# Kernel tuning notes

Hardware: AMD Instinct MI355X
Metric: run time of the kernel (lower is better)

The kernel has to match this reference:

```python
import jax, jax.numpy as jnp
import numpy as np
from jax import lax
import math

B, CH, BINS, CROP = 8, 2, 1024, 1024
NUM_BANDS = 4
FF = 2048
EPS = 1e-5
SCALE = 0.02  # weight init scale for numeric stability


def _inorm(x, g, b):
    # InstanceNorm2d: x [B, C, H, W], normalize over (H, W) per (B, C); biased var
    m = x.mean(axis=(2, 3), keepdims=True)
    v = x.var(axis=(2, 3), keepdims=True)
    return (x - m) / jnp.sqrt(v + EPS) * g[None, :, None, None] + b[None, :, None, None]


def _dwconv(x, k):
    # depthwise conv1d: x [B, bins, W], k [bins, 1, 3], padding=1, groups=bins
    return lax.conv_general_dilated(x, k, (1,), [(1, 1)],
                                    dimension_numbers=('NCH', 'OIH', 'NCH'),
                                    feature_group_count=x.shape[1])


def setup_inputs() -> dict:
    key = jax.random.key(0)
    ks = jax.random.split(key, 12)
    inp = {
        'x': jax.random.normal(ks[0], (B, CH, BINS, CROP), jnp.float32),
        'prev_qk': jax.random.normal(ks[1], (B, NUM_BANDS, CROP, CROP), jnp.float32),
        'g_in': jnp.ones((CROP,), jnp.float32),
        'b_in': jnp.zeros((CROP,), jnp.float32),
        'W_in': jax.random.normal(ks[2], (1, CH), jnp.float32) * SCALE,
        'bias_in': jnp.zeros((1,), jnp.float32),
        'g1': jnp.ones((CROP,), jnp.float32),
        'b1': jnp.zeros((CROP,), jnp.float32),
        'Wq': jax.random.normal(ks[3], (BINS, BINS), jnp.float32) * SCALE,
        'Wk': jax.random.normal(ks[4], (BINS, BINS), jnp.float32) * SCALE,
        'Wv': jax.random.normal(ks[5], (BINS, BINS), jnp.float32) * SCALE,
        'Wo': jax.random.normal(ks[6], (BINS, BINS), jnp.float32) * SCALE,
        'kq': jax.random.normal(ks[7], (BINS, 1, 3), jnp.float32) * SCALE,
        'kk': jax.random.normal(ks[8], (BINS, 1, 3), jnp.float32) * SCALE,
        'kv': jax.random.normal(ks[9], (BINS, 1, 3), jnp.float32) * SCALE,
        'pos_w': jax.random.normal(ks[10], (BINS // NUM_BANDS, CROP), jnp.float32) * SCALE,
        'g2': jnp.ones((CROP,), jnp.float32),
        'b2': jnp.zeros((CROP,), jnp.float32),
        'W_ff': jax.random.normal(ks[11], (1, 2), jnp.float32) * SCALE,
        'bias_ff': jnp.zeros((1,), jnp.float32),
        'W1': jax.random.normal(jax.random.fold_in(key, 100), (FF, BINS), jnp.float32) * SCALE,
        'W2': jax.random.normal(jax.random.fold_in(key, 101), (BINS, FF), jnp.float32) * SCALE,
    }
    return inp


def reference(x, prev_qk, g_in, b_in, W_in, bias_in, g1, b1, Wq, Wk, Wv, Wo,
              kq, kk, kv, pos_w, g2, b2, W_ff, bias_ff, W1, W2):
    b = x.shape[0]
    nb = NUM_BANDS
    hd = BINS // nb
    # in_norm + in_project: transposed layout [B, CROP, BINS, CH]
    xt = jnp.transpose(x, (0, 3, 2, 1))
    xt = _inorm(xt, g_in, b_in)
    xt = jnp.einsum('bwhc,oc->bwho', xt, W_in) + bias_in  # [B,CROP,BINS,1]
    x0 = jnp.transpose(xt, (0, 3, 2, 1))                  # [B,1,BINS,CROP]
    # norm1 + attention over frames (w == CROP, c == BINS)
    h = jnp.transpose(_inorm(jnp.transpose(x0, (0, 3, 2, 1)), g1, b1), (0, 3, 2, 1))
    a_in = jnp.transpose(h, (0, 3, 2, 1))[..., 0]         # [B, W, BINS]
    q = jnp.einsum('bwc,oc->bwo', a_in, Wq)
    q = jnp.transpose(_dwconv(jnp.transpose(q, (0, 2, 1)), kq), (0, 2, 1))
    k = jnp.einsum('bwc,oc->bwo', a_in, Wk)
    k = jnp.transpose(_dwconv(jnp.transpose(k, (0, 2, 1)), kk), (0, 2, 1))
    v = jnp.einsum('bwc,oc->bwo', a_in, Wv)
    v = jnp.transpose(_dwconv(jnp.transpose(v, (0, 2, 1)), kv), (0, 2, 1))
    q4 = jnp.transpose(q.reshape(b, CROP, nb, hd), (0, 2, 1, 3))   # [B,nb,W,hd]
    k4 = jnp.transpose(k.reshape(b, CROP, nb, hd), (0, 2, 3, 1))   # [B,nb,hd,W]
    v4 = jnp.transpose(v.reshape(b, CROP, nb, hd), (0, 2, 1, 3))   # [B,nb,W,hd]
    # relative-position bias via pad-and-shift
    p = jnp.matmul(q4, pos_w)                                      # [B,nb,W,CROP]
    p = jnp.pad(p, ((0, 0), (0, 0), (0, 0), (1, 0)))
    p = jnp.swapaxes(p, 2, 3)[:, :, 1:, :]                         # [B,nb,CROP,W]
    qk = (jnp.matmul(q4, k4) + p) / math.sqrt(BINS)
    qk = qk + prev_qk
    a = jax.nn.softmax(qk, axis=-1)
    o = jnp.transpose(jnp.matmul(a, v4), (0, 2, 1, 3)).reshape(b, CROP, BINS)
    o = jnp.einsum('bwc,oc->bwo', o, Wo)                           # [B,W,BINS]
    h4 = jnp.transpose(o[..., None], (0, 3, 2, 1))                 # [B,1,BINS,CROP]
    x1 = jnp.concatenate([x0, h4], axis=1)                         # [B,2,BINS,CROP]
    # norm2 + ff_project + squared-ReLU FFN
    hn = _inorm(jnp.transpose(x1, (0, 3, 2, 1)), g2, b2)           # [B,CROP,BINS,2]
    hn = jnp.einsum('bwhc,oc->bwho', hn, W_ff) + bias_ff           # [B,CROP,BINS,1]
    hn = jnp.transpose(hn, (0, 3, 2, 1))                           # [B,1,BINS,CROP]
    ht = jnp.swapaxes(hn, 2, 3)                                    # [B,1,CROP,BINS]
    ht = jnp.square(jax.nn.relu(jnp.einsum('bowc,fc->bowf', ht, W1)))
    ht = jnp.einsum('bowf,cf->bowc', ht, W2)
    hf = jnp.swapaxes(ht, 2, 3)                                    # [B,1,BINS,CROP]
    out = jnp.concatenate([x1, hf], axis=1)                        # [B,3,BINS,CROP]
    return out, qk
```

## Files before the change

### kernel.cpp

```cpp
#include <hip/hip_runtime.h>
#include <stdint.h>

#define DEVI __device__ __forceinline__

typedef __attribute__((ext_vector_type(8))) short bf16x8;
typedef __attribute__((ext_vector_type(4))) float f32x4;

#define B_    8
#define CROP_ 1024
#define BINS_ 1024
#define NB_   4
#define HD_   256
#define FF_   2048
#define EPSF  1e-5f
#define OUT0_ELEMS (8ull*3ull*1024ull*1024ull)
#define MBYTE (1024ull*1024ull)
#define M1ELEM (1024ll*1024ll)
#define SMCAP 8.0f

DEVI unsigned short f2bf(float f) {
  unsigned u = __builtin_bit_cast(unsigned, f);
  u += 0x7fffu + ((u >> 16) & 1u);
  return (unsigned short)(u >> 16);
}
DEVI float bf2f(unsigned short h) {
  unsigned u = ((unsigned)h) << 16;
  return __builtin_bit_cast(float, u);
}

DEVI void gload16(const unsigned short* g, unsigned short* l) {
  __builtin_amdgcn_global_load_lds(
      (const __attribute__((address_space(1))) unsigned int*)g,
      (__attribute__((address_space(3))) unsigned int*)l, 16, 0, 0);
}

__global__ __launch_bounds__(256) void k_conv_all(
    const float* __restrict__ Wq, const float* __restrict__ Wk,
    const float* __restrict__ Wv, const float* __restrict__ Wo,
    const float* __restrict__ W1, const float* __restrict__ W2,
    const float* __restrict__ pw,
    unsigned short* __restrict__ WQKVB, unsigned short* __restrict__ WOB,
    unsigned short* __restrict__ W1B, unsigned short* __restrict__ W2B,
    unsigned short* __restrict__ PWT) {
  long long i = (long long)blockIdx.x*256 + threadIdx.x;
  long long stride = (long long)gridDim.x*256;
  const long long total = 8*M1ELEM + (1 << 18);
  for (; i < total; i += stride) {
    if (i < 3*M1ELEM) {
      const float* s = i < M1ELEM ? Wq : (i < 2*M1ELEM ? Wk : Wv);
      WQKVB[i] = f2bf(s[i & (M1ELEM-1)]);
    } else if (i < 4*M1ELEM) { WOB[i-3*M1ELEM] = f2bf(Wo[i-3*M1ELEM]); }
    else if (i < 6*M1ELEM)   { W1B[i-4*M1ELEM] = f2bf(W1[i-4*M1ELEM]); }
    else if (i < 8*M1ELEM)   { W2B[i-6*M1ELEM] = f2bf(W2[i-6*M1ELEM]); }
    else {
      long long j = i - 8*M1ELEM;
      int w = (int)(j >> 8), d = (int)(j & 255);
      PWT[j] = f2bf(pw[d*1024 + w]);
    }
  }
}

__global__ __launch_bounds__(256) void k_instx0(const float* __restrict__ x,
    const float* __restrict__ g_in, const float* __restrict__ b_in,
    const float* __restrict__ W_in, const float* __restrict__ bias_in,
    const float* __restrict__ g1, const float* __restrict__ b1,
    float* __restrict__ outp, float* __restrict__ x0t,
    unsigned short* __restrict__ ain) {
  int b = blockIdx.y, w0 = blockIdx.x*32;
  int t = threadIdx.x, wl = t & 31, p = t >> 5;
  const float* xb = x + (size_t)b*2*M1ELEM + w0 + wl;
  float s = 0.f, ss = 0.f;
  for (int i = p*256; i < p*256 + 256; ++i) {
    float v = xb[(size_t)i*CROP_];
    s += v; ss += v*v;
  }
  __shared__ float ls[8][32], lss[8][32];
  __shared__ float s_coef[32], s_add[32];
  __shared__ float s_cm[32], s_ca[32];
  ls[p][wl] = s; lss[p][wl] = ss;
  __syncthreads();
  float W0 = W_in[0], W1 = W_in[1], bi = bias_in[0];
  float sW = W0 + W1;
  if (t < 32) {
    float S = 0.f, SS = 0.f;
    for (int q = 0; q < 8; ++q) { S += ls[q][t]; SS += lss[q][t]; }
    float m = S*(1.f/2048.f);
    float var = SS*(1.f/2048.f) - m*m;
    float r = rsqrtf(var + EPSF);
    int w = w0 + t;
    float coef = r*g_in[w];
    s_coef[t] = coef;
    s_add[t] = b_in[w]*sW + bi - coef*m*sW;
  }
  __syncthreads();
  __shared__ float tile[32][33];
  int tx = wl, ty = p;
  float coef = s_coef[tx], add = s_add[tx];
  int w = w0 + tx;
  float s1 = 0.f, ss1 = 0.f;
  for (int h0 = 0; h0 < BINS_; h0 += 32) {
#pragma unroll
    for (int q = 0; q < 4; ++q) {
      int h = h0 + ty + q*8;
      size_t i0 = ((size_t)b*2*BINS_ + h)*CROP_ + w;
      float val = coef*(W0*x[i0] + W1*x[i0 + (size_t)M1ELEM]) + add;
      outp[(((size_t)b*3)*BINS_ + h)*CROP_ + w] = val;
      tile[ty + q*8][tx] = val;
      s1 += val; ss1 += val*val;
    }
    __syncthreads();
#pragma unroll
    for (int q = 0; q < 4; ++q)
      x0t[((size_t)b*CROP_ + w0 + ty + q*8)*BINS_ + h0 + tx] = tile[tx][ty + q*8];
    __syncthreads();
  }
  ls[p][wl] = s1; lss[p][wl] = ss1;
  __syncthreads();
  if (t < 32) {
    float S = 0.f, SS = 0.f;
    for (int q = 0; q < 8; ++q) { S += ls[q][t]; SS += lss[q][t]; }
    float m = S*(1.f/1024.f);
    float var = SS*(1.f/1024.f) - m*m;
    float rs = rsqrtf(var + EPSF);
    int ww = w0 + t;
    float cm = rs*g1[ww];
    s_cm[t] = cm;
    s_ca[t] = b1[ww] - m*cm;
  }
  __syncthreads();
  for (int wloc = 0; wloc < 32; ++wloc) {
    float cm = s_cm[wloc], ca = s_ca[wloc];
    const float* row = x0t + ((size_t)b*CROP_ + w0 + wloc)*BINS_;
    float4 v = *(const float4*)&row[t*4];
    ushort4 o;
    o.x = f2bf(v.x*cm + ca);
    o.y = f2bf(v.y*cm + ca);
    o.z = f2bf(v.z*cm + ca);
    o.w = f2bf(v.w*cm + ca);
    *(ushort4*)&ain[((size_t)b*CROP_ + w0 + wloc)*BINS_ + t*4] = o;
  }
}

__global__ __launch_bounds__(256) void k_norm2(const float* __restrict__ x0t,
    const float* __restrict__ o2,
    const float* __restrict__ g2, const float* __restrict__ b2,
    const float* __restrict__ W_ff, const float* __restrict__ bias_ff,
    unsigned short* __restrict__ hn) {
  int r = blockIdx.x;
  int w = r & (CROP_ - 1);
  int t = threadIdx.x;
  const float* ra = x0t + (size_t)r*BINS_;
  const float* rb = o2 + (size_t)r*BINS_;
  float va[4], vb[4], s = 0.f, ss = 0.f;
  for (int q = 0; q < 4; ++q) {
    va[q] = ra[t + q*256]; vb[q] = rb[t + q*256];
    s += va[q] + vb[q]; ss += va[q]*va[q] + vb[q]*vb[q];
  }
  for (int off = 32; off; off >>= 1) { s += __shfl_xor(s, off); ss += __shfl_xor(ss, off); }
  __shared__ float red[8];
  int wv = t >> 6;
  if ((t & 63) == 0) { red[wv] = s; red[4 + wv] = ss; }
  __syncthreads();
  s = red[0] + red[1] + red[2] + red[3];
  ss = red[4] + red[5] + red[6] + red[7];
  float m = s*(1.f/2048.f);
  float var = ss*(1.f/2048.f) - m*m;
  float rs = rsqrtf(var + EPSF);
  float W0 = W_ff[0], W1f = W_ff[1];
  float gg = g2[w]*rs;
  float add = b2[w]*(W0 + W1f) + bias_ff[0];
  for (int q = 0; q < 4; ++q)
    hn[(size_t)r*BINS_ + t + q*256] = f2bf(gg*(W0*(va[q] - m) + W1f*(vb[q] - m)) + add);
}

__global__ __launch_bounds__(256) void k_dwconv(const unsigned short* __restrict__ qkvb,
    const float* __restrict__ kq, const float* __restrict__ kk2,
    unsigned short* __restrict__ qkvc) {
  int w = blockIdx.x, b = blockIdx.y, which = blockIdx.z;
  int t = threadIdx.x;
  const float* kw = which == 0 ? kq : kk2;
  const unsigned short* r0 = qkvb + (size_t)which*8*M1ELEM + ((size_t)b*CROP_ + w)*BINS_;
  unsigned short* d0 = qkvc + (size_t)which*8*M1ELEM + ((size_t)b*CROP_ + w)*BINS_;
  int c4 = t*4;
  float kf[12];
  *(float4*)&kf[0] = *(const float4*)&kw[c4*3];
  *(float4*)&kf[4] = *(const float4*)&kw[c4*3 + 4];
  *(float4*)&kf[8] = *(const float4*)&kw[c4*3 + 8];
  ushort4 vm = *(const ushort4*)&r0[c4];
  ushort4 va = make_ushort4(0,0,0,0), vbn = make_ushort4(0,0,0,0);
  if (w > 0)        va  = *(const ushort4*)&r0[c4 - BINS_];
  if (w < CROP_-1)  vbn = *(const ushort4*)&r0[c4 + BINS_];
  const unsigned short* vmp = (const unsigned short*)&vm;
  const unsigned short* vap = (const unsigned short*)&va;
  const unsigned short* vbp = (const unsigned short*)&vbn;
  ushort4 o;
  unsigned short* op = (unsigned short*)&o;
#pragma unroll
  for (int j = 0; j < 4; ++j) {
    float acc = bf2f(vmp[j])*kf[3*j + 1] + bf2f(vap[j])*kf[3*j] + bf2f(vbp[j])*kf[3*j + 2];
    op[j] = f2bf(acc);
  }
  *(ushort4*)&d0[c4] = o;
}

__global__ __launch_bounds__(256) void k_dwconv_trV(const unsigned short* __restrict__ vb,
    const float* __restrict__ kv, unsigned short* __restrict__ vct) {
  int b = blockIdx.z;
  int w0 = blockIdx.x*32, c0 = blockIdx.y*32;
  int tx = threadIdx.x, ty = threadIdx.y;
  __shared__ unsigned short tile[34][33];
  const unsigned short* S = vb + (size_t)b*M1ELEM;
#pragma unroll
  for (int q = 0; q < 4; ++q) {
    int wl = ty + q*8;
    tile[wl + 1][tx] = S[(size_t)(w0 + wl)*BINS_ + c0 + tx];
  }
  if (ty == 0) tile[0][tx]  = (w0 > 0)          ? S[(size_t)(w0 - 1)*BINS_ + c0 + tx] : (unsigned short)0;
  if (ty == 1) tile[33][tx] = (w0 + 32 < CROP_) ? S[(size_t)(w0 + 32)*BINS_ + c0 + tx] : (unsigned short)0;
  __syncthreads();
  unsigned short* D = vct + (size_t)b*M1ELEM;
#pragma unroll
  for (int q = 0; q < 4; ++q) {
    int cl = ty + q*8;
    int c = c0 + cl;
    float k0 = kv[c*3], k1 = kv[c*3 + 1], k2 = kv[c*3 + 2];
    float val = k0*bf2f(tile[tx][cl]) + k1*bf2f(tile[tx + 1][cl]) + k2*bf2f(tile[tx + 2][cl]);
    D[(size_t)c*CROP_ + w0 + tx] = f2bf(val);
  }
}

#define BUFB 49152

template<int AC, int BC, int ABY>
DEVI void stage_gen(const unsigned short* Ab, int lda, const unsigned short* Bb, int ldb,
                    int k0, unsigned short* buf, int t, int wv) {
  int trow = t >> 3;
  int colel = ((t & 7) ^ (trow & 7)) << 3;
  unsigned short* lbase = buf + wv*512;
  const unsigned short* ga = Ab + (size_t)trow*lda + k0 + colel;
#pragma unroll
  for (int c = 0; c < AC; ++c)
    gload16(ga + (size_t)(c*64)*lda, lbase + c*4096);
  const unsigned short* gb = Bb + (size_t)trow*ldb + k0 + colel;
  unsigned short* lbb = buf + ABY/2 + wv*512;
#pragma unroll
  for (int c = 0; c < BC; ++c)
    gload16(gb + (size_t)(c*64)*ldb, lbb + c*4096);
}

#define RING_BODY(BOFF, ...)                                                           \
    bf16x8 af[2][4], bf[2][4];                                                         \
    _Pragma("unroll")                                                                  \
    for (int kk = 0; kk < 2; ++kk) {                                                   \
      _Pragma("unroll")                                                                \
      for (int mi = 0; mi < 4; ++mi) {                                                 \
        int row = wm*64 + mi*16 + lr;                                                  \
        af[kk][mi] = *(const bf16x8*)(bufc + ((row*128 + kk*64 + lk*16) ^ sx));        \
      }                                                                                \
      _Pragma("unroll")                                                                \
      for (int ni = 0; ni < 4; ++ni) {                                                 \
        int row = wn*64 + ni*16 + lr;                                                  \
        bf[kk][ni] = *(const bf16x8*)(bufc + BOFF + ((row*128 + kk*64 + lk*16) ^ sx)); \
      }                                                                                \
    }                                                                                  \
    asm volatile("s_waitcnt lgkmcnt(0)" ::: "memory");                                 \
    __builtin_amdgcn_s_barrier();                                                      \
    __VA_ARGS__;                                                                       \
    __builtin_amdgcn_s_setprio(1);                                                     \
    _Pragma("unroll")                                                                  \
    for (int kk = 0; kk < 2; ++kk)                                                     \
      _Pragma("unroll")                                                                \
      for (int mi = 0; mi < 4; ++mi)                                                   \
        _Pragma("unroll")                                                              \
        for (int ni = 0; ni < 4; ++ni)                                                 \
          acc[mi][ni] = __builtin_amdgcn_mfma_f32_16x16x32_bf16(af[kk][mi], bf[kk][ni], acc[mi][ni], 0, 0, 0); \
    __builtin_amdgcn_s_setprio(0);                                                     \
    if (kt + 1 < NT) {                                                                 \
      int rem = (NT-1 < kt+3 ? NT-1 : kt+3) - (kt+1);                                  \
      if (rem >= 2)      asm volatile("s_waitcnt vmcnt(12)" ::: "memory");             \
      else if (rem == 1) asm volatile("s_waitcnt vmcnt(6)"  ::: "memory");             \
      else               asm volatile("s_waitcnt vmcnt(0)"  ::: "memory");             \
      __builtin_amdgcn_s_barrier();                                                    \
    }

template<int MODE>
__global__ __launch_bounds__(512) void k_gemm3(
    const unsigned short* __restrict__ A, int lda,
    const unsigned short* __restrict__ Bt, int ldb,
    void* __restrict__ C, int ldc, int K, float* __restrict__ C2, int ch)
{
  __shared__ __align__(16) unsigned short lds[3*24576];
  const unsigned short* Ab = A + (size_t)blockIdx.x*256*lda;
  const unsigned short* Bb = Bt + (size_t)blockIdx.y*128*ldb;
  const int t = threadIdx.x;
  const int wv = t >> 6, ln = t & 63;
  const int wm = wv >> 1, wn = wv & 1;
  const int lr = ln & 15, lk = ln >> 4;
  const int sx = (lr & 7) << 4;
  const int NT = K >> 6;
  stage_gen<4,2,32768>(Ab, lda, Bb, ldb, 0,   lds,           t, wv);
  stage_gen<4,2,32768>(Ab, lda, Bb, ldb, 64,  lds + 24576,   t, wv);
  stage_gen<4,2,32768>(Ab, lda, Bb, ldb, 128, lds + 49152,   t, wv);
  asm volatile("s_waitcnt vmcnt(12)" ::: "memory");
  __builtin_amdgcn_s_barrier();

  f32x4 acc[4][4] = {};
  for (int kt = 0; kt < NT; ++kt) {
    const int cur = kt % 3;
    const char* bufc = (const char*)lds + cur*BUFB;
    RING_BODY(32768,
      if (kt + 3 < NT) stage_gen<4,2,32768>(Ab, lda, Bb, ldb, (kt+3)*64,
                                            (unsigned short*)((char*)lds + cur*BUFB), t, wv))
  }

  if (MODE != 3) {
    const int row0 = blockIdx.x*256 + wm*64 + lk*4;
    const int col0 = blockIdx.y*128 + wn*64 + lr;
#pragma unroll
    for (int mi = 0; mi < 4; ++mi)
#pragma unroll
      for (int ni = 0; ni < 4; ++ni)
#pragma unroll
        for (int j = 0; j < 4; ++j) {
          int row = row0 + mi*16 + j;
          int col = col0 + ni*16;
          float v = acc[mi][ni][j];
          if (MODE == 0 || MODE == 4) {
            ((float*)C)[(size_t)row*ldc + col] = v;
          } else if (MODE == 2) {
            float rr = fmaxf(v, 0.f);
            ((unsigned short*)C)[(size_t)row*ldc + col] = f2bf(rr*rr);
          } else if (MODE == 5) {
            ((unsigned short*)C)[(size_t)(col >> 10)*8*M1ELEM + (size_t)row*1024 + (col & 1023)] = f2bf(v);
          }
        }
  }
  if (MODE == 3 || MODE == 4) {
    __syncthreads();
    float* ldsT = (float*)lds + wv*4160;
#pragma unroll
    for (int mi = 0; mi < 4; ++mi)
#pragma unroll
      for (int ni = 0; ni < 4; ++ni)
#pragma unroll
        for (int j = 0; j < 4; ++j)
          ldsT[(ni*16 + lr)*65 + mi*16 + lk*4 + j] = acc[mi][ni][j];
    asm volatile("s_waitcnt lgkmcnt(0)" ::: "memory");
    int l16 = ln & 15, csub = ln >> 4;
    int b = blockIdx.x >> 2;
    int wbase = ((blockIdx.x & 3) << 8) + wm*64 + l16*4;
    float* outc = C2 + (((size_t)b*3 + ch)*BINS_)*CROP_;
#pragma unroll
    for (int cb = 0; cb < 16; ++cb) {
      int cl = cb*4 + csub;
      float4 v4;
      v4.x = ldsT[cl*65 + l16*4 + 0];
      v4.y = ldsT[cl*65 + l16*4 + 1];
      v4.z = ldsT[cl*65 + l16*4 + 2];
      v4.w = ldsT[cl*65 + l16*4 + 3];
      *(float4*)&outc[(size_t)(blockIdx.y*128 + wn*64 + cl)*CROP_ + wbase] = v4;
    }
  }
}

DEVI void stage_qk(const unsigned short* qc_b, const unsigned short* kc_b,
                   const unsigned short* pwt, int bx, int by, int k0,
                   unsigned short* buf, int t, int wv) {
  int trow = t >> 3;
  int colel = ((t & 7) ^ (trow & 7)) << 3;
  unsigned short* lbase = buf + wv*512;
  if (k0 < 256) {
    const unsigned short* ga = qc_b + (size_t)(bx*256 + trow)*BINS_ + k0 + colel;
#pragma unroll
    for (int c = 0; c < 4; ++c)
      gload16(ga + (size_t)(c*64)*BINS_, lbase + c*4096);
  } else {
    const unsigned short* ga = pwt + (size_t)(bx*256 + trow)*HD_ + (k0 - 256) + colel;
#pragma unroll
    for (int c = 0; c < 4; ++c)
      gload16(ga + (size_t)(c*64)*HD_, lbase + c*4096);
  }
  const unsigned short* gbsrc = (k0 < 256) ? kc_b : qc_b;
  int kb = (k0 < 256) ? k0 : k0 - 256;
  const unsigned short* gb = gbsrc + (size_t)(by*128 + trow)*BINS_ + kb + colel;
  unsigned short* lbb = buf + 16384 + wv*512;
#pragma unroll
  for (int c = 0; c < 2; ++c)
    gload16(gb + (size_t)(c*64)*BINS_, lbb + c*4096);
}

__global__ __launch_bounds__(512) void k_qkpos2(
    const unsigned short* __restrict__ qc, const unsigned short* __restrict__ kc,
    const unsigned short* __restrict__ pwt,
    const float* __restrict__ prev, float* __restrict__ qkout,
    unsigned short* __restrict__ Pbuf, float* __restrict__ Lg)
{
  __shared__ __align__(16) unsigned short lds[3*24576];
  const int z = blockIdx.z, b = z >> 2, n = z & 3;
  const size_t bandoff = (size_t)b*CROP_*BINS_ + (size_t)n*HD_;
  const unsigned short* qc_b = qc + bandoff;
  const unsigned short* kc_b = kc + bandoff;
  const int bx = blockIdx.x, by = blockIdx.y;
  const int t = threadIdx.x;
  const int wv = t >> 6, ln = t & 63;
  const int wm = wv >> 1, wn = wv & 1;
  const int lr = ln & 15, lk = ln >> 4;
  const int sx = (lr & 7) << 4;
  const int NT = 8;
  stage_qk(qc_b, kc_b, pwt, bx, by, 0,   lds,         t, wv);
  stage_qk(qc_b, kc_b, pwt, bx, by, 64,  lds + 24576, t, wv);
  stage_qk(qc_b, kc_b, pwt, bx, by, 128, lds + 49152, t, wv);
  asm volatile("s_waitcnt vmcnt(12)" ::: "memory");
  __builtin_amdgcn_s_barrier();

  f32x4 acc[4][4] = {};
  for (int kt = 0; kt < NT; ++kt) {
    const int cur = kt % 3;
    const char* bufc = (const char*)lds + cur*BUFB;
    RING_BODY(32768,
      if (kt + 3 < NT) stage_qk(qc_b, kc_b, pwt, bx, by, (kt+3)*64,
                                (unsigned short*)((char*)lds + cur*BUFB), t, wv))
  }

  const float* pz = prev + (size_t)z*M1ELEM;
  float* oz = qkout + (size_t)z*M1ELEM;
  unsigned short* Pz = Pbuf + (size_t)z*M1ELEM;
  const int row0g = bx*256;
  const int col0 = by*128 + wn*64 + lr;
  float* slf = (float*)lds;
  const int rbase = wm*64 + lk*4;
#pragma unroll
  for (int mi = 0; mi < 4; ++mi) {
    float psum[4] = {0.f, 0.f, 0.f, 0.f};
#pragma unroll
    for (int ni = 0; ni < 4; ++ni)
#pragma unroll
      for (int j = 0; j < 4; ++j) {
        size_t idx = (size_t)(row0g + rbase + mi*16 + j)*CROP_ + col0 + ni*16;
        float val = acc[mi][ni][j]*0.03125f + pz[idx];
        oz[idx] = val;
        float p = __expf(val - SMCAP);
        Pz[idx] = f2bf(p);
        psum[j] += p;
      }
#pragma unroll
    for (int off = 1; off < 16; off <<= 1)
#pragma unroll
      for (int j = 0; j < 4; ++j) psum[j] += __shfl_xor(psum[j], off);
    if (lr == 0)
#pragma unroll
      for (int j = 0; j < 4; ++j) slf[wn*256 + rbase + mi*16 + j] = psum[j];
  }
  __syncthreads();
  if (t < 256) {
    size_t si = ((size_t)z*CROP_ + row0g + t)*8 + by;
    Lg[si] = slf[t] + slf[256 + t];
  }
}

__global__ __launch_bounds__(512) void k_pv3(
    const unsigned short* __restrict__ P, const float* __restrict__ Lg,
    const unsigned short* __restrict__ vct, unsigned short* __restrict__ ob)
{
  __shared__ __align__(16) unsigned short lds[3*24576];
  __shared__ float s_il[128];
  const int z = blockIdx.y, b = z >> 2, band = z & 3;
  const int bx = blockIdx.x;
  const unsigned short* Ab = P + (size_t)z*M1ELEM + (size_t)bx*128*CROP_;
  const unsigned short* Bb = vct + ((size_t)b*CROP_ + band*HD_)*CROP_;
  const int t = threadIdx.x;
  const int wv = t >> 6, ln = t & 63;
  const int wm = wv >> 2, wn = wv & 3;
  const int lr = ln & 15, lk = ln >> 4;
  const int sx = (lr & 7) << 4;
  const int NT = 16;
  if (t < 128) {
    size_t rg = (size_t)z*CROP_ + bx*128 + t;
    float l = 0.f;
#pragma unroll
    for (int cb = 0; cb < 8; ++cb) l += Lg[rg*8 + cb];
    s_il[t] = 1.f / l;
  }
  stage_gen<2,4,16384>(Ab, CROP_, Bb, CROP_, 0,   lds,         t, wv);
  stage_gen<2,4,16384>(Ab, CROP_, Bb, CROP_, 64,  lds + 24576, t, wv);
  stage_gen<2,4,16384>(Ab, CROP_, Bb, CROP_, 128, lds + 49152, t, wv);
  asm volatile("s_waitcnt vmcnt(12) lgkmcnt(0)" ::: "memory");
  __builtin_amdgcn_s_barrier();

  f32x4 acc[4][4] = {};
  for (int kt = 0; kt < NT; ++kt) {
    const int cur = kt % 3;
    const char* bufc = (const char*)lds + cur*BUFB;
    RING_BODY(16384,
      if (kt + 3 < NT) stage_gen<2,4,16384>(Ab, CROP_, Bb, CROP_, (kt+3)*64,
                                            (unsigned short*)((char*)lds + cur*BUFB), t, wv))
  }
#pragma unroll
  for (int mi = 0; mi < 4; ++mi)
#pragma unroll
    for (int j = 0; j < 4; ++j) {
      int rl = wm*64 + mi*16 + lk*4 + j;
      float il = s_il[rl];
#pragma unroll
      for (int ni = 0; ni < 4; ++ni) {
        int col = band*HD_ + wn*64 + ni*16 + lr;
        ob[((size_t)b*CROP_ + bx*128 + rl)*BINS_ + col] = f2bf(acc[mi][ni][j]*il);
      }
    }
}

extern "C" void kernel_launch(void* const* d_in, const int* in_sizes, int n_in,
                              void* d_out, int out_size, void* d_ws, size_t ws_size,
                              hipStream_t stream) {
  (void)in_sizes; (void)n_in; (void)out_size; (void)ws_size;
  const float* x       = (const float*)d_in[0];
  const float* prev_qk = (const float*)d_in[1];
  const float* g_in    = (const float*)d_in[2];
  const float* b_in    = (const float*)d_in[3];
  const float* W_in    = (const float*)d_in[4];
  const float* bias_in = (const float*)d_in[5];
  const float* g1      = (const float*)d_in[6];
  const float* b1      = (const float*)d_in[7];
  const float* Wq      = (const float*)d_in[8];
  const float* Wk      = (const float*)d_in[9];
  const float* Wv      = (const float*)d_in[10];
  const float* Wo      = (const float*)d_in[11];
  const float* kq      = (const float*)d_in[12];
  const float* kk      = (const float*)d_in[13];
  const float* kv      = (const float*)d_in[14];
  const float* pos_w   = (const float*)d_in[15];
  const float* g2      = (const float*)d_in[16];
  const float* b2      = (const float*)d_in[17];
  const float* W_ff    = (const float*)d_in[18];
  const float* bias_ff = (const float*)d_in[19];
  const float* W1      = (const float*)d_in[20];
  const float* W2      = (const float*)d_in[21];

  char* ws = (char*)d_ws;
  unsigned short* WQKVB = (unsigned short*)(ws + 0*MBYTE);
  unsigned short* WOB   = (unsigned short*)(ws + 6*MBYTE);
  unsigned short* W1B   = (unsigned short*)(ws + 8*MBYTE);
  unsigned short* W2B   = (unsigned short*)(ws + 12*MBYTE);
  unsigned short* PWT   = (unsigned short*)(ws + 16*MBYTE);
  float*          Lg    = (float*)(ws + 17*MBYTE);
  float*          X0T   = (float*)(ws + 20*MBYTE);
  unsigned short* AIN   = (unsigned short*)(ws + 52*MBYTE);
  unsigned short* QKVB  = (unsigned short*)(ws + 68*MBYTE);
  unsigned short* PBUF  = (unsigned short*)(ws + 52*MBYTE);
  unsigned short* QKVC  = (unsigned short*)(ws + 116*MBYTE);
  float*          O2    = (float*)(ws + 116*MBYTE);
  unsigned short* OB    = (unsigned short*)(ws + 148*MBYTE);
  unsigned short* VCT   = (unsigned short*)(ws + 164*MBYTE);
  unsigned short* HN    = (unsigned short*)(ws + 52*MBYTE);
  unsigned short* HT    = (unsigned short*)(ws + 20*MBYTE);

  float* outp  = (float*)d_out;
  float* qkout = outp + OUT0_ELEMS;

  dim3 blk256(256, 1, 1);
  dim3 blk512(512, 1, 1);
  dim3 blk32x8(32, 8, 1);

  k_conv_all<<<8448, blk256, 0, stream>>>(Wq, Wk, Wv, Wo, W1, W2, pos_w,
                                          WQKVB, WOB, W1B, W2B, PWT);
  k_instx0<<<dim3(32, 8, 1), blk256, 0, stream>>>(x, g_in, b_in, W_in, bias_in,
                                                  g1, b1, outp, X0T, AIN);
  k_gemm3<5><<<dim3(32, 24, 1), blk512, 0, stream>>>(AIN, 1024, WQKVB, 1024, QKVB, 0, 1024, nullptr, 0);
  k_dwconv<<<dim3(1024, 8, 2), blk256, 0, stream>>>(QKVB, kq, kk, QKVC);
  k_dwconv_trV<<<dim3(32, 32, 8), blk32x8, 0, stream>>>(QKVB + (size_t)2*8*M1ELEM, kv, VCT);
  k_qkpos2<<<dim3(4, 8, 32), blk512, 0, stream>>>(QKVC, QKVC + (size_t)8*M1ELEM, PWT,
                                                  prev_qk, qkout, PBUF, Lg);
  k_pv3<<<dim3(8, 32, 1), blk512, 0, stream>>>(PBUF, Lg, VCT, OB);
  k_gemm3<4><<<dim3(32, 8, 1), blk512, 0, stream>>>(OB, 1024, WOB, 1024, O2, 1024, 1024, outp, 1);
  k_norm2<<<8192, blk256, 0, stream>>>(X0T, O2, g2, b2, W_ff, bias_ff, HN);
  k_gemm3<2><<<dim3(32, 16, 1), blk512, 0, stream>>>(HN, 1024, W1B, 1024, HT, 2048, 1024, nullptr, 0);
  k_gemm3<3><<<dim3(32, 8, 1), blk512, 0, stream>>>(HT, 2048, W2B, 2048, nullptr, 1024, 2048, outp, 2);
}
```

Measured before the change: 450.9 us.

## Use 256x256 double-buffered GEMM tiles for QKV, FFN1 and QK^T kernels

Adds a k_gemm4 kernel with 256x256 output tiles, 8 waves arranged 2x4, each computing 128x64, and a two-stage LDS double buffer. It replaces the 256x128 triple-buffered kernel for the QKV projection and the first FFN GEMM. The QK^T+pos+softmax-stats kernel is rewritten the same way, which halves the number of column blocks and per-row partial sums (Lg now holds 4 partials instead of 8). The goal is more operand reuse per LDS load and less global traffic, at the cost of higher register pressure (32 accumulators per thread), fewer blocks, and only two pipeline stages.

Result: slower. 578.1 us (+28.2%).

```diff
diff --git a/kernel.cpp b/kernel.cpp
--- a/kernel.cpp
+++ b/kernel.cpp
@@ -283,6 +283,39 @@
       __builtin_amdgcn_s_barrier();                                                    \
     }
 
+#define RING_BODY4(BOFF, ...)                                                          \
+    bf16x8 af[2][8], bf[2][4];                                                         \
+    _Pragma("unroll")                                                                  \
+    for (int kk = 0; kk < 2; ++kk) {                                                   \
+      _Pragma("unroll")                                                                \
+      for (int mi = 0; mi < 8; ++mi) {                                                 \
+        int row = wm*128 + mi*16 + lr;                                                 \
+        af[kk][mi] = *(const bf16x8*)(bufc + ((row*128 + kk*64 + lk*16) ^ sx));        \
+      }                                                                                \
+      _Pragma("unroll")                                                                \
+      for (int ni = 0; ni < 4; ++ni) {                                                 \
+        int row = wn*64 + ni*16 + lr;                                                  \
+        bf[kk][ni] = *(const bf16x8*)(bufc + BOFF + ((row*128 + kk*64 + lk*16) ^ sx)); \
+      }                                                                                \
+    }                                                                                  \
+    asm volatile("s_waitcnt lgkmcnt(0)" ::: "memory");                                 \
+    __builtin_amdgcn_s_barrier();                                                      \
+    __VA_ARGS__;                                                                       \
+    __builtin_amdgcn_s_setprio(1);                                                     \
+    _Pragma("unroll")                                                                  \
+    for (int kk = 0; kk < 2; ++kk)                                                     \
+      _Pragma("unroll")                                                                \
+      for (int mi = 0; mi < 8; ++mi)                                                   \
+        _Pragma("unroll")                                                              \
+        for (int ni = 0; ni < 4; ++ni)                                                 \
+          acc[mi][ni] = __builtin_amdgcn_mfma_f32_16x16x32_bf16(af[kk][mi], bf[kk][ni], acc[mi][ni], 0, 0, 0); \
+    __builtin_amdgcn_s_setprio(0);                                                     \
+    if (kt + 1 < NT) {                                                                 \
+      if (kt + 2 < NT) asm volatile("s_waitcnt vmcnt(8)" ::: "memory");                \
+      else             asm volatile("s_waitcnt vmcnt(0)" ::: "memory");                \
+      __builtin_amdgcn_s_barrier();                                                    \
+    }
+
 template<int MODE>
 __global__ __launch_bounds__(512) void k_gemm3(
     const unsigned short* __restrict__ A, int lda,
@@ -324,15 +357,7 @@
         for (int j = 0; j < 4; ++j) {
           int row = row0 + mi*16 + j;
           int col = col0 + ni*16;
-          float v = acc[mi][ni][j];
-          if (MODE == 0 || MODE == 4) {
-            ((float*)C)[(size_t)row*ldc + col] = v;
-          } else if (MODE == 2) {
-            float rr = fmaxf(v, 0.f);
-            ((unsigned short*)C)[(size_t)row*ldc + col] = f2bf(rr*rr);
-          } else if (MODE == 5) {
-            ((unsigned short*)C)[(size_t)(col >> 10)*8*M1ELEM + (size_t)row*1024 + (col & 1023)] = f2bf(v);
-          }
+          ((float*)C)[(size_t)row*ldc + col] = acc[mi][ni][j];
         }
   }
   if (MODE == 3 || MODE == 4) {
@@ -363,9 +388,57 @@
   }
 }
 
-DEVI void stage_qk(const unsigned short* qc_b, const unsigned short* kc_b,
-                   const unsigned short* pwt, int bx, int by, int k0,
-                   unsigned short* buf, int t, int wv) {
+template<int MODE>
+__global__ __launch_bounds__(512) void k_gemm4(
+    const unsigned short* __restrict__ A, int lda,
+    const unsigned short* __restrict__ Bt, int ldb,
+    void* __restrict__ C, int ldc, int K)
+{
+  __shared__ __align__(16) unsigned short lds[65536];
+  const unsigned short* Ab = A + (size_t)blockIdx.x*256*lda;
+  const unsigned short* Bb = Bt + (size_t)blockIdx.y*256*ldb;
+  const int t = threadIdx.x;
+  const int wv = t >> 6, ln = t & 63;
+  const int wm = wv >> 2, wn = wv & 3;
+  const int lr = ln & 15, lk = ln >> 4;
+  const int sx = (lr & 7) << 4;
+  const int NT = K >> 6;
+  stage_gen<4,4,32768>(Ab, lda, Bb, ldb, 0,  lds,         t, wv);
+  stage_gen<4,4,32768>(Ab, lda, Bb, ldb, 64, lds + 32768, t, wv);
+  asm volatile("s_waitcnt vmcnt(8)" ::: "memory");
+  __builtin_amdgcn_s_barrier();
+
+  f32x4 acc[8][4] = {};
+  for (int kt = 0; kt < NT; ++kt) {
+    const char* bufc = (const char*)lds + (kt & 1)*65536;
+    RING_BODY4(32768,
+      if (kt + 2 < NT) stage_gen<4,4,32768>(Ab, lda, Bb, ldb, (kt+2)*64,
+                                            (unsigned short*)((char*)lds + (kt&1)*65536), t, wv))
+  }
+
+  const int row0 = blockIdx.x*256 + wm*128 + lk*4;
+  const int col0 = blockIdx.y*256 + wn*64 + lr;
+#pragma unroll
+  for (int mi = 0; mi < 8; ++mi)
+#pragma unroll
+    for (int ni = 0; ni < 4; ++ni)
+#pragma unroll
+      for (int j = 0; j < 4; ++j) {
+        int row = row0 + mi*16 + j;
+        int col = col0 + ni*16;
+        float v = acc[mi][ni][j];
+        if (MODE == 2) {
+          float rr = fmaxf(v, 0.f);
+          ((unsigned short*)C)[(size_t)row*ldc + col] = f2bf(rr*rr);
+        } else {
+          ((unsigned short*)C)[(size_t)(col >> 10)*8*M1ELEM + (size_t)row*1024 + (col & 1023)] = f2bf(v);
+        }
+      }
+}
+
+DEVI void stage_qk4(const unsigned short* qc_b, const unsigned short* kc_b,
+                    const unsigned short* pwt, int bx, int by, int k0,
+                    unsigned short* buf, int t, int wv) {
   int trow = t >> 3;
   int colel = ((t & 7) ^ (trow & 7)) << 3;
   unsigned short* lbase = buf + wv*512;
@@ -382,20 +455,20 @@
   }
   const unsigned short* gbsrc = (k0 < 256) ? kc_b : qc_b;
   int kb = (k0 < 256) ? k0 : k0 - 256;
-  const unsigned short* gb = gbsrc + (size_t)(by*128 + trow)*BINS_ + kb + colel;
+  const unsigned short* gb = gbsrc + (size_t)(by*256 + trow)*BINS_ + kb + colel;
   unsigned short* lbb = buf + 16384 + wv*512;
 #pragma unroll
-  for (int c = 0; c < 2; ++c)
+  for (int c = 0; c < 4; ++c)
     gload16(gb + (size_t)(c*64)*BINS_, lbb + c*4096);
 }
 
-__global__ __launch_bounds__(512) void k_qkpos2(
+__global__ __launch_bounds__(512) void k_qkpos4(
     const unsigned short* __restrict__ qc, const unsigned short* __restrict__ kc,
     const unsigned short* __restrict__ pwt,
     const float* __restrict__ prev, float* __restrict__ qkout,
     unsigned short* __restrict__ Pbuf, float* __restrict__ Lg)
 {
-  __shared__ __align__(16) unsigned short lds[3*24576];
+  __shared__ __align__(16) unsigned short lds[65536];
   const int z = blockIdx.z, b = z >> 2, n = z & 3;
   const size_t bandoff = (size_t)b*CROP_*BINS_ + (size_t)n*HD_;
   const unsigned short* qc_b = qc + bandoff;
@@ -403,34 +476,32 @@
   const int bx = blockIdx.x, by = blockIdx.y;
   const int t = threadIdx.x;
   const int wv = t >> 6, ln = t & 63;
-  const int wm = wv >> 1, wn = wv & 1;
+  const int wm = wv >> 2, wn = wv & 3;
   const int lr = ln & 15, lk = ln >> 4;
   const int sx = (lr & 7) << 4;
   const int NT = 8;
-  stage_qk(qc_b, kc_b, pwt, bx, by, 0,   lds,         t, wv);
-  stage_qk(qc_b, kc_b, pwt, bx, by, 64,  lds + 24576, t, wv);
-  stage_qk(qc_b, kc_b, pwt, bx, by, 128, lds + 49152, t, wv);
-  asm volatile("s_waitcnt vmcnt(12)" ::: "memory");
+  stage_qk4(qc_b, kc_b, pwt, bx, by, 0,  lds,         t, wv);
+  stage_qk4(qc_b, kc_b, pwt, bx, by, 64, lds + 32768, t, wv);
+  asm volatile("s_waitcnt vmcnt(8)" ::: "memory");
   __builtin_amdgcn_s_barrier();
 
-  f32x4 acc[4][4] = {};
+  f32x4 acc[8][4] = {};
   for (int kt = 0; kt < NT; ++kt) {
-    const int cur = kt % 3;
-    const char* bufc = (const char*)lds + cur*BUFB;
-    RING_BODY(32768,
-      if (kt + 3 < NT) stage_qk(qc_b, kc_b, pwt, bx, by, (kt+3)*64,
-                                (unsigned short*)((char*)lds + cur*BUFB), t, wv))
+    const char* bufc = (const char*)lds + (kt & 1)*65536;
+    RING_BODY4(32768,
+      if (kt + 2 < NT) stage_qk4(qc_b, kc_b, pwt, bx, by, (kt+2)*64,
+                                 (unsigned short*)((char*)lds + (kt&1)*65536), t, wv))
   }
 
   const float* pz = prev + (size_t)z*M1ELEM;
   float* oz = qkout + (size_t)z*M1ELEM;
   unsigned short* Pz = Pbuf + (size_t)z*M1ELEM;
   const int row0g = bx*256;
-  const int col0 = by*128 + wn*64 + lr;
+  const int col0 = by*256 + wn*64 + lr;
   float* slf = (float*)lds;
-  const int rbase = wm*64 + lk*4;
-#pragma unroll
-  for (int mi = 0; mi < 4; ++mi) {
+  const int rbase = wm*128 + lk*4;
+#pragma unroll
+  for (int mi = 0; mi < 8; ++mi) {
     float psum[4] = {0.f, 0.f, 0.f, 0.f};
 #pragma unroll
     for (int ni = 0; ni < 4; ++ni)
@@ -453,8 +524,8 @@
   }
   __syncthreads();
   if (t < 256) {
-    size_t si = ((size_t)z*CROP_ + row0g + t)*8 + by;
-    Lg[si] = slf[t] + slf[256 + t];
+    size_t si = ((size_t)z*CROP_ + row0g + t)*4 + by;
+    Lg[si] = slf[t] + slf[256 + t] + slf[512 + t] + slf[768 + t];
   }
 }
 
@@ -478,7 +549,7 @@
     size_t rg = (size_t)z*CROP_ + bx*128 + t;
     float l = 0.f;
 #pragma unroll
-    for (int cb = 0; cb < 8; ++cb) l += Lg[rg*8 + cb];
+    for (int cb = 0; cb < 4; ++cb) l += Lg[rg*4 + cb];
     s_il[t] = 1.f / l;
   }
   stage_gen<2,4,16384>(Ab, CROP_, Bb, CROP_, 0,   lds,         t, wv);
@@ -565,14 +636,14 @@
                                           WQKVB, WOB, W1B, W2B, PWT);
   k_instx0<<<dim3(32, 8, 1), blk256, 0, stream>>>(x, g_in, b_in, W_in, bias_in,
                                                   g1, b1, outp, X0T, AIN);
-  k_gemm3<5><<<dim3(32, 24, 1), blk512, 0, stream>>>(AIN, 1024, WQKVB, 1024, QKVB, 0, 1024, nullptr, 0);
+  k_gemm4<5><<<dim3(32, 12, 1), blk512, 0, stream>>>(AIN, 1024, WQKVB, 1024, QKVB, 0, 1024);
   k_dwconv<<<dim3(1024, 8, 2), blk256, 0, stream>>>(QKVB, kq, kk, QKVC);
   k_dwconv_trV<<<dim3(32, 32, 8), blk32x8, 0, stream>>>(QKVB + (size_t)2*8*M1ELEM, kv, VCT);
-  k_qkpos2<<<dim3(4, 8, 32), blk512, 0, stream>>>(QKVC, QKVC + (size_t)8*M1ELEM, PWT,
+  k_qkpos4<<<dim3(4, 4, 32), blk512, 0, stream>>>(QKVC, QKVC + (size_t)8*M1ELEM, PWT,
                                                   prev_qk, qkout, PBUF, Lg);
   k_pv3<<<dim3(8, 32, 1), blk512, 0, stream>>>(PBUF, Lg, VCT, OB);
   k_gemm3<4><<<dim3(32, 8, 1), blk512, 0, stream>>>(OB, 1024, WOB, 1024, O2, 1024, 1024, outp, 1);
   k_norm2<<<8192, blk256, 0, stream>>>(X0T, O2, g2, b2, W_ff, bias_ff, HN);
-  k_gemm3<2><<<dim3(32, 16, 1), blk512, 0, stream>>>(HN, 1024, W1B, 1024, HT, 2048, 1024, nullptr, 0);
+  k_gemm4<2><<<dim3(32, 8, 1), blk512, 0, stream>>>(HN, 1024, W1B, 1024, HT, 2048, 1024);
   k_gemm3<3><<<dim3(32, 8, 1), blk512, 0, stream>>>(HT, 2048, W2B, 2048, nullptr, 1024, 2048, outp, 2);
 }
```
